# Performance work log

Measured on AMD Instinct MI355X. Metric: run time of the kernel, lower is better.

## Reference

```python
import jax, jax.numpy as jnp
import numpy as np

V, E, H, N, L = 32000, 512, 512, 64, 128


def setup_inputs() -> dict:
    key = jax.random.key(0)
    ks = jax.random.split(key, 16)
    s = 0.02  # init scale
    return {
        "input_ids": jax.random.randint(ks[0], (N,), 0, V),
        "h": jax.random.normal(ks[1], (N, H), jnp.float32),
        "c": jax.random.normal(ks[2], (N, H), jnp.float32),
        "encoder_hiddens": jax.random.normal(ks[3], (N, L, H), jnp.float32),
        "attn_mask": jnp.zeros((N, L), dtype=bool),
        "embed_W": jax.random.normal(ks[4], (V, E), jnp.float32) * s,
        "w_ih": jax.random.normal(ks[5], (4 * H, E), jnp.float32) * s,
        "b_ih": jnp.zeros((4 * H,), jnp.float32),
        "w_hh": jax.random.normal(ks[6], (4 * H, H), jnp.float32) * s,
        "b_hh": jnp.zeros((4 * H,), jnp.float32),
        "attn_Wh": jax.random.normal(ks[7], (H, H), jnp.float32) * s,
        "attn_Ws": jax.random.normal(ks[8], (H, H), jnp.float32) * s,
        "attn_v": jax.random.normal(ks[9], (H,), jnp.float32) * s,
        "h2o_W": jax.random.normal(ks[10], (V, 2 * H), jnp.float32) * s,
        "h2o_b": jnp.zeros((V,), jnp.float32),
    }


def reference(input_ids, h, c, encoder_hiddens, attn_mask, embed_W,
              w_ih, b_ih, w_hh, b_hh, attn_Wh, attn_Ws, attn_v,
              h2o_W, h2o_b):
    # Embedding lookup: (N, E)
    emb = embed_W[input_ids]
    # LSTM cell: fused gate GEMMs, chunk order i, f, g, o (torch chunk(4))
    gates = emb @ w_ih.T + b_ih + h @ w_hh.T + b_hh  # (N, 4H)
    i_g, f_g, g_g, o_g = jnp.split(gates, 4, axis=1)
    c_t = jax.nn.sigmoid(f_g) * c + jax.nn.sigmoid(i_g) * jnp.tanh(g_g)
    h_t = jax.nn.sigmoid(o_g) * jnp.tanh(c_t)  # (N, H)
    # Bahdanau attention: v^T tanh(W_h h_t + W_s enc)
    proj = jnp.tanh((h_t @ attn_Wh.T)[:, None, :] + encoder_hiddens @ attn_Ws.T)  # (N, L, H)
    score = jnp.einsum('nlh,h->nl', proj, attn_v)  # (N, L)
    score = jnp.where(attn_mask, -jnp.inf, score)
    attn_w = jax.nn.softmax(score, axis=1)  # (N, L)
    context = jnp.einsum('nl,nlh->nh', attn_w, encoder_hiddens)  # (N, H)
    # Output projection + log-softmax over vocab
    combined = jnp.concatenate([h_t, context], axis=1)  # (N, 2H)
    out = jax.nn.log_softmax(combined @ h2o_W.T + h2o_b, axis=-1)  # (N, V)
    return out, h_t, c_t
```

## Files before the change

kernel.cpp:

```cpp
#include <hip/hip_runtime.h>
#include <math.h>

#define V 32000
#define E 512
#define H 512
#define N 64
#define L 128
#define NV (N*V)
#define NH (N*H)
#define MTOT (N*L)
#define VT 500

typedef short  s8v  __attribute__((ext_vector_type(8)));
typedef float  f4v  __attribute__((ext_vector_type(4)));

__device__ __forceinline__ float sigf(float x) { return 1.0f / (1.0f + __expf(-x)); }

__device__ __forceinline__ unsigned short f2bf(float f) {
    unsigned int u = __float_as_uint(f);
    unsigned int r = u + 0x7FFFu + ((u >> 16) & 1u);
    return (unsigned short)(r >> 16);
}

__global__ __launch_bounds__(256) void k_gates(
    const int* __restrict__ ids, const float* __restrict__ hprev,
    const float* __restrict__ embW, const float* __restrict__ w_ih,
    const float* __restrict__ w_hh, float* __restrict__ gates_p)
{
    __shared__ __align__(16) float xs[64 * 128];
    const int bx = blockIdx.x;
    const int ks = blockIdx.y;
    const int tid = threadIdx.x;
    const bool emb_part = (ks < 4);
    const int koff = (ks & 3) * 128;

    for (int i = tid; i < 64 * 32; i += 256) {
        int n = i >> 5, kk4 = i & 31;
        float4 x4;
        if (emb_part)
            x4 = ((const float4*)(embW + (size_t)ids[n] * E + koff))[kk4];
        else
            x4 = ((const float4*)(hprev + (size_t)n * H + koff))[kk4];
        ((float4*)xs)[n * 32 + kk4] = x4;
    }
    __syncthreads();

    const int jl = tid & 63;
    const int ng = tid >> 6;
    const int j = bx * 64 + jl;
    const int nb = ng * 16;
    const float* wrow = (emb_part ? w_ih : w_hh) + (size_t)j * 512 + koff;

    float acc[16];
#pragma unroll
    for (int i = 0; i < 16; ++i) acc[i] = 0.f;

    for (int e4 = 0; e4 < 32; ++e4) {
        float4 w4 = ((const float4*)wrow)[e4];
#pragma unroll
        for (int i = 0; i < 16; ++i) {
            float4 x4 = ((const float4*)xs)[(nb + i) * 32 + e4];
            acc[i] += w4.x * x4.x + w4.y * x4.y + w4.z * x4.z + w4.w * x4.w;
        }
    }
#pragma unroll
    for (int i = 0; i < 16; ++i)
        gates_p[(size_t)ks * (64 * 2048) + (size_t)(nb + i) * 2048 + j] = acc[i];
}

__global__ __launch_bounds__(256) void k_lstm_pw(
    const float* __restrict__ gates_p, const float* __restrict__ b_ih,
    const float* __restrict__ b_hh, const float* __restrict__ cprev,
    float* __restrict__ out, unsigned short* __restrict__ xb)
{
    int i = blockIdx.x * 256 + threadIdx.x;
    if (i >= NH) return;
    int n = i >> 9, k = i & 511;
    float g[4];
#pragma unroll
    for (int q = 0; q < 4; ++q) {
        int j = q * 512 + k;
        float s = b_ih[j] + b_hh[j];
#pragma unroll
        for (int ks = 0; ks < 8; ++ks)
            s += gates_p[(size_t)ks * (64 * 2048) + (size_t)n * 2048 + j];
        g[q] = s;
    }
    float ig = sigf(g[0]), fg = sigf(g[1]), gg = tanhf(g[2]), og = sigf(g[3]);
    float ct = fg * cprev[i] + ig * gg;
    float ht = og * tanhf(ct);
    out[NV + i] = ht;
    out[NV + NH + i] = ct;
    xb[(size_t)n * 1024 + k] = f2bf(ht);
}

__global__ __launch_bounds__(256) void k_sproj(
    const float* __restrict__ out, const float* __restrict__ Wh,
    float* __restrict__ sproj)
{
    __shared__ __align__(16) float xs[512];
    int n = blockIdx.x >> 1;
    int h = (blockIdx.x & 1) * 256 + threadIdx.x;
    const float* ht = out + NV + (size_t)n * 512;
    for (int i = threadIdx.x; i < 512; i += 256) xs[i] = ht[i];
    __syncthreads();
    const float* wrow = Wh + (size_t)h * 512;
    float acc = 0.f;
    for (int e4 = 0; e4 < 128; ++e4) {
        float4 w4 = ((const float4*)wrow)[e4];
        float4 x4 = ((const float4*)xs)[e4];
        acc += w4.x * x4.x + w4.y * x4.y + w4.z * x4.z + w4.w * x4.w;
    }
    sproj[(size_t)n * 512 + h] = acc;
}

__global__ __launch_bounds__(256) void k_score_gemm(
    const float* __restrict__ enc, const float* __restrict__ Ws,
    const float* __restrict__ sproj, const float* __restrict__ av,
    float* __restrict__ scorep)
{
    __shared__ __align__(16) short As[64 * 72];
    __shared__ __align__(16) short Bs[64 * 72];
    __shared__ float sred[64];

    const int bm = blockIdx.x, bh = blockIdx.y;
    const int tid = threadIdx.x;
    const int w = tid >> 6, l = tid & 63;
    const int wave_m = (w >> 1) * 32, wave_h = (w & 1) * 32;
    const int lq = l >> 4, lr = l & 15;

    if (tid < 64) sred[tid] = 0.f;

    f4v acc[2][2];
#pragma unroll
    for (int i = 0; i < 2; ++i)
#pragma unroll
        for (int j = 0; j < 2; ++j) acc[i][j] = (f4v)0.f;

    for (int kt = 0; kt < 8; ++kt) {
        __syncthreads();
#pragma unroll
        for (int r = 0; r < 2; ++r) {
            int idx = (r * 256 + tid) * 8;
            int row = idx >> 6, col = idx & 63;
            const float* sa = enc + (size_t)(bm * 64 + row) * 512 + kt * 64 + col;
            const float* sb = Ws  + (size_t)(bh * 64 + row) * 512 + kt * 64 + col;
            float4 a0 = *(const float4*)sa, a1 = *(const float4*)(sa + 4);
            float4 b0 = *(const float4*)sb, b1 = *(const float4*)(sb + 4);
            union { unsigned short u[8]; uint4 q; } pa, pb;
            pa.u[0]=f2bf(a0.x); pa.u[1]=f2bf(a0.y); pa.u[2]=f2bf(a0.z); pa.u[3]=f2bf(a0.w);
            pa.u[4]=f2bf(a1.x); pa.u[5]=f2bf(a1.y); pa.u[6]=f2bf(a1.z); pa.u[7]=f2bf(a1.w);
            pb.u[0]=f2bf(b0.x); pb.u[1]=f2bf(b0.y); pb.u[2]=f2bf(b0.z); pb.u[3]=f2bf(b0.w);
            pb.u[4]=f2bf(b1.x); pb.u[5]=f2bf(b1.y); pb.u[6]=f2bf(b1.z); pb.u[7]=f2bf(b1.w);
            *(uint4*)(As + row * 72 + col) = pa.q;
            *(uint4*)(Bs + row * 72 + col) = pb.q;
        }
        __syncthreads();

#pragma unroll
        for (int ks = 0; ks < 2; ++ks) {
            s8v a_frag[2], b_frag[2];
#pragma unroll
            for (int i = 0; i < 2; ++i)
                a_frag[i] = *(const s8v*)(As + (wave_m + 16 * i + lr) * 72 + ks * 32 + lq * 8);
#pragma unroll
            for (int j = 0; j < 2; ++j)
                b_frag[j] = *(const s8v*)(Bs + (wave_h + 16 * j + lr) * 72 + ks * 32 + lq * 8);
#pragma unroll
            for (int i = 0; i < 2; ++i)
#pragma unroll
                for (int j = 0; j < 2; ++j)
                    acc[i][j] = __builtin_amdgcn_mfma_f32_16x16x32_bf16(
                        a_frag[i], b_frag[j], acc[i][j], 0, 0, 0);
        }
    }
    __syncthreads();

    const int hc0 = bh * 64 + wave_h + lr;
#pragma unroll
    for (int i = 0; i < 2; ++i) {
#pragma unroll
        for (int reg = 0; reg < 4; ++reg) {
            int m_local = wave_m + 16 * i + lq * 4 + reg;
            int m = bm * 64 + m_local;
            int n = m >> 7;
            float p = 0.f;
#pragma unroll
            for (int j = 0; j < 2; ++j) {
                int hc = hc0 + 16 * j;
                float val = acc[i][j][reg] + sproj[(size_t)n * 512 + hc];
                p += tanhf(val) * av[hc];
            }
            p += __shfl_xor(p, 1, 64);
            p += __shfl_xor(p, 2, 64);
            p += __shfl_xor(p, 4, 64);
            p += __shfl_xor(p, 8, 64);
            if (lr == 0) atomicAdd(&sred[m_local], p);
        }
    }
    __syncthreads();
    if (tid < 64)
        scorep[(size_t)bh * MTOT + bm * 64 + tid] = sred[tid];
}

__global__ __launch_bounds__(512) void k_softmax_ctx(
    const float* __restrict__ scorep, const unsigned char* __restrict__ mask,
    const float* __restrict__ enc, unsigned short* __restrict__ xb)
{
    __shared__ float sc[128];
    __shared__ float wl[128];
    const int n = blockIdx.x, t = threadIdx.x;

    if (t < 128) {
        float s = 0.f;
#pragma unroll
        for (int q = 0; q < 8; ++q)
            s += scorep[(size_t)q * MTOT + n * 128 + t];
        if (mask[(size_t)n * 128 + t]) s = -1e30f;
        sc[t] = s;
    }
    __syncthreads();
    if (t < 64) {
        float m = fmaxf(sc[t], sc[t + 64]);
#pragma unroll
        for (int off = 32; off > 0; off >>= 1) m = fmaxf(m, __shfl_xor(m, off, 64));
        float e0 = __expf(sc[t] - m), e1 = __expf(sc[t + 64] - m);
        float ss = e0 + e1;
#pragma unroll
        for (int off = 32; off > 0; off >>= 1) ss += __shfl_xor(ss, off, 64);
        float inv = 1.0f / ss;
        wl[t] = e0 * inv;
        wl[t + 64] = e1 * inv;
    }
    __syncthreads();

    const float* encn = enc + (size_t)n * L * H + t;
    float acc = 0.f;
#pragma unroll 4
    for (int ll = 0; ll < 128; ++ll)
        acc += wl[ll] * encn[(size_t)ll * 512];
    xb[(size_t)n * 1024 + 512 + t] = f2bf(acc);
}

__global__ __launch_bounds__(256) void k_logits(
    const float* __restrict__ h2oW, const unsigned short* __restrict__ xb,
    const float* __restrict__ h2ob, float* __restrict__ dlogits,
    float* __restrict__ pmax, float* __restrict__ psum)
{
    __shared__ __align__(16) short As[64 * 72];
    __shared__ __align__(16) short Bs[64 * 72];
    __shared__ __align__(16) float cs[64 * 68];

    const int bm = blockIdx.x;
    const int tid = threadIdx.x;
    const int w = tid >> 6, l = tid & 63;
    const int wave_m = (w & 1) * 32, wave_n = (w >> 1) * 32;
    const int lq = l >> 4, lr = l & 15;

    const int arow = tid >> 2;
    const int acol = (tid & 3) * 16;
    const float* aptr = h2oW + (size_t)(bm * 64 + arow) * 1024 + acol;
    const unsigned short* bptr = xb + (size_t)arow * 1024 + acol;

    f4v acc[2][2];
#pragma unroll
    for (int i = 0; i < 2; ++i)
#pragma unroll
        for (int j = 0; j < 2; ++j) acc[i][j] = (f4v)0.f;

    float4 ra[4];
    uint4  rb[2];
#pragma unroll
    for (int r = 0; r < 4; ++r) ra[r] = ((const float4*)aptr)[r];
    rb[0] = *(const uint4*)bptr;
    rb[1] = *(const uint4*)(bptr + 8);

#pragma unroll 1
    for (int kt = 0; kt < 16; ++kt) {
        if (kt) __syncthreads();
        union { unsigned short u[8]; uint4 q; } p0, p1;
        p0.u[0]=f2bf(ra[0].x); p0.u[1]=f2bf(ra[0].y); p0.u[2]=f2bf(ra[0].z); p0.u[3]=f2bf(ra[0].w);
        p0.u[4]=f2bf(ra[1].x); p0.u[5]=f2bf(ra[1].y); p0.u[6]=f2bf(ra[1].z); p0.u[7]=f2bf(ra[1].w);
        p1.u[0]=f2bf(ra[2].x); p1.u[1]=f2bf(ra[2].y); p1.u[2]=f2bf(ra[2].z); p1.u[3]=f2bf(ra[2].w);
        p1.u[4]=f2bf(ra[3].x); p1.u[5]=f2bf(ra[3].y); p1.u[6]=f2bf(ra[3].z); p1.u[7]=f2bf(ra[3].w);
        *(uint4*)(As + arow * 72 + acol)     = p0.q;
        *(uint4*)(As + arow * 72 + acol + 8) = p1.q;
        *(uint4*)(Bs + arow * 72 + acol)     = rb[0];
        *(uint4*)(Bs + arow * 72 + acol + 8) = rb[1];
        __syncthreads();

        if (kt < 15) {
            const float* ap = aptr + (kt + 1) * 64;
            const unsigned short* bp = bptr + (kt + 1) * 64;
#pragma unroll
            for (int r = 0; r < 4; ++r) ra[r] = ((const float4*)ap)[r];
            rb[0] = *(const uint4*)bp;
            rb[1] = *(const uint4*)(bp + 8);
        }

#pragma unroll
        for (int ks = 0; ks < 2; ++ks) {
            s8v a_frag[2], b_frag[2];
#pragma unroll
            for (int i = 0; i < 2; ++i)
                a_frag[i] = *(const s8v*)(As + (wave_m + 16 * i + lr) * 72 + ks * 32 + lq * 8);
#pragma unroll
            for (int j = 0; j < 2; ++j)
                b_frag[j] = *(const s8v*)(Bs + (wave_n + 16 * j + lr) * 72 + ks * 32 + lq * 8);
#pragma unroll
            for (int i = 0; i < 2; ++i)
#pragma unroll
                for (int j = 0; j < 2; ++j)
                    acc[i][j] = __builtin_amdgcn_mfma_f32_16x16x32_bf16(
                        a_frag[i], b_frag[j], acc[i][j], 0, 0, 0);
        }
    }
    __syncthreads();

#pragma unroll
    for (int i = 0; i < 2; ++i)
#pragma unroll
        for (int j = 0; j < 2; ++j)
#pragma unroll
            for (int reg = 0; reg < 4; ++reg)
                cs[(wave_n + 16 * j + lr) * 68 + wave_m + 16 * i + lq * 4 + reg] = acc[i][j][reg];
    __syncthreads();

    const int n = tid >> 2, q = tid & 3;
    const int v0 = bm * 64 + q * 16;
    float4 vals[4];
    float m_loc = -1e30f;
#pragma unroll
    for (int k = 0; k < 4; ++k) {
        float4 cv = *(const float4*)(cs + n * 68 + q * 16 + 4 * k);
        float4 bv = *(const float4*)(h2ob + v0 + 4 * k);
        cv.x += bv.x; cv.y += bv.y; cv.z += bv.z; cv.w += bv.w;
        vals[k] = cv;
        *(float4*)(dlogits + (size_t)n * V + v0 + 4 * k) = cv;
        m_loc = fmaxf(m_loc, fmaxf(fmaxf(cv.x, cv.y), fmaxf(cv.z, cv.w)));
    }
    float s_loc = 0.f;
#pragma unroll
    for (int k = 0; k < 4; ++k) {
        s_loc += __expf(vals[k].x - m_loc) + __expf(vals[k].y - m_loc)
               + __expf(vals[k].z - m_loc) + __expf(vals[k].w - m_loc);
    }
    float m2 = fmaxf(m_loc, __shfl_xor(m_loc, 1, 64));
    m2 = fmaxf(m2, __shfl_xor(m2, 2, 64));
    s_loc *= __expf(m_loc - m2);
    float s2 = s_loc + __shfl_xor(s_loc, 1, 64);
    s2 += __shfl_xor(s2, 2, 64);
    if (q == 0) {
        pmax[(size_t)n * VT + bm] = m2;
        psum[(size_t)n * VT + bm] = s2;
    }
}

__global__ __launch_bounds__(256) void k_lse(
    const float* __restrict__ pmax, const float* __restrict__ psum,
    float* __restrict__ lse)
{
    __shared__ float rm[4], rs[4];
    const int n = blockIdx.x, t = threadIdx.x;
    float m0 = (t < VT) ? pmax[(size_t)n * VT + t] : -1e30f;
    float m1 = (t + 256 < VT) ? pmax[(size_t)n * VT + t + 256] : -1e30f;
    float mm = fmaxf(m0, m1);
#pragma unroll
    for (int off = 32; off > 0; off >>= 1) mm = fmaxf(mm, __shfl_xor(mm, off, 64));
    if ((t & 63) == 0) rm[t >> 6] = mm;
    __syncthreads();
    float m = fmaxf(fmaxf(rm[0], rm[1]), fmaxf(rm[2], rm[3]));

    float s = 0.f;
    if (t < VT)       s += psum[(size_t)n * VT + t] * __expf(m0 - m);
    if (t + 256 < VT) s += psum[(size_t)n * VT + t + 256] * __expf(m1 - m);
#pragma unroll
    for (int off = 32; off > 0; off >>= 1) s += __shfl_xor(s, off, 64);
    if ((t & 63) == 0) rs[t >> 6] = s;
    __syncthreads();
    if (t == 0) {
        float st = rs[0] + rs[1] + rs[2] + rs[3];
        lse[n] = m + __logf(st);
    }
}

__global__ __launch_bounds__(256) void k_norm(
    float* __restrict__ dlogits, const float* __restrict__ lse)
{
    const int n = blockIdx.y;
    const int t4 = blockIdx.x * 256 + threadIdx.x;
    if (t4 >= V / 4) return;
    float s = lse[n];
    float4* p = (float4*)(dlogits + (size_t)n * V) + t4;
    float4 v = *p;
    v.x -= s; v.y -= s; v.z -= s; v.w -= s;
    *p = v;
}

extern "C" void kernel_launch(void* const* d_in, const int* in_sizes, int n_in,
                              void* d_out, int out_size, void* d_ws, size_t ws_size,
                              hipStream_t stream)
{
    const int* ids   = (const int*)d_in[0];
    const float* h   = (const float*)d_in[1];
    const float* c   = (const float*)d_in[2];
    const float* enc = (const float*)d_in[3];
    const unsigned char* mask = (const unsigned char*)d_in[4];
    const float* embW = (const float*)d_in[5];
    const float* w_ih = (const float*)d_in[6];
    const float* b_ih = (const float*)d_in[7];
    const float* w_hh = (const float*)d_in[8];
    const float* b_hh = (const float*)d_in[9];
    const float* Wh   = (const float*)d_in[10];
    const float* Ws   = (const float*)d_in[11];
    const float* av   = (const float*)d_in[12];
    const float* h2oW = (const float*)d_in[13];
    const float* h2ob = (const float*)d_in[14];

    float* out = (float*)d_out;
    float* ws = (float*)d_ws;
    float* gates_p = ws;
    float* sproj   = ws + 1048576;
    float* scorep  = ws + 1048576 + 32768;
    unsigned short* xb = (unsigned short*)(ws + 1048576 + 32768 + 65536);
    float* pmax = ws;
    float* psum = ws + 32000;
    float* lse  = ws + 64000;

    k_gates<<<dim3(32, 8), 256, 0, stream>>>(ids, h, embW, w_ih, w_hh, gates_p);
    k_lstm_pw<<<128, 256, 0, stream>>>(gates_p, b_ih, b_hh, c, out, xb);
    k_sproj<<<128, 256, 0, stream>>>(out, Wh, sproj);
    k_score_gemm<<<dim3(128, 8), 256, 0, stream>>>(enc, Ws, sproj, av, scorep);
    k_softmax_ctx<<<64, 512, 0, stream>>>(scorep, mask, enc, xb);
    k_logits<<<VT, 256, 0, stream>>>(h2oW, xb, h2ob, out, pmax, psum);
    k_lse<<<64, 256, 0, stream>>>(pmax, psum, lse);
    k_norm<<<dim3(32, 64), 256, 0, stream>>>(out, lse);
}
```

Before: 348.9 us.

## Split-K logits GEMM, wider softmax-ctx grid, packed bf16 convert, swapped score grid

The logits kernel now uses 512 threads in two groups, each handling half of K with its own LDS tiles, and their partial accumulators are summed in shared memory. The register prefetch of the next tile is dropped. The softmax/context kernel is spread over a 64x4 grid of 128-thread blocks, and the score GEMM grid is transposed so consecutive blocks share an encoder tile. Scalar float-to-bf16 rounding is replaced with the paired __float22bfloat162_rn conversion. The aim is more parallelism per block and cheaper conversions, at the cost of losing load/compute overlap in the logits GEMM and adding an extra reduction step.

After: 342.4 us. Within noise of the previous version (-1.9%).

```diff
diff --git a/kernel.cpp b/kernel.cpp
--- a/kernel.cpp
+++ b/kernel.cpp
@@ -1,4 +1,5 @@
 #include <hip/hip_runtime.h>
+#include <hip/hip_bf16.h>
 #include <math.h>
 
 #define V 32000
@@ -22,6 +23,20 @@
     return (unsigned short)(r >> 16);
 }
 
+__device__ __forceinline__ unsigned int cvt2bf(float x, float y) {
+    __hip_bfloat162 h2 = __float22bfloat162_rn(make_float2(x, y));
+    unsigned int r;
+    __builtin_memcpy(&r, &h2, 4);
+    return r;
+}
+
+__device__ __forceinline__ uint4 pack_q(float4 lo, float4 hi) {
+    uint4 q;
+    q.x = cvt2bf(lo.x, lo.y); q.y = cvt2bf(lo.z, lo.w);
+    q.z = cvt2bf(hi.x, hi.y); q.w = cvt2bf(hi.z, hi.w);
+    return q;
+}
+
 __global__ __launch_bounds__(256) void k_gates(
     const int* __restrict__ ids, const float* __restrict__ hprev,
     const float* __restrict__ embW, const float* __restrict__ w_ih,
@@ -123,7 +138,7 @@
     __shared__ __align__(16) short Bs[64 * 72];
     __shared__ float sred[64];
 
-    const int bm = blockIdx.x, bh = blockIdx.y;
+    const int bh = blockIdx.x, bm = blockIdx.y;
     const int tid = threadIdx.x;
     const int w = tid >> 6, l = tid & 63;
     const int wave_m = (w >> 1) * 32, wave_h = (w & 1) * 32;
@@ -147,13 +162,8 @@
             const float* sb = Ws  + (size_t)(bh * 64 + row) * 512 + kt * 64 + col;
             float4 a0 = *(const float4*)sa, a1 = *(const float4*)(sa + 4);
             float4 b0 = *(const float4*)sb, b1 = *(const float4*)(sb + 4);
-            union { unsigned short u[8]; uint4 q; } pa, pb;
-            pa.u[0]=f2bf(a0.x); pa.u[1]=f2bf(a0.y); pa.u[2]=f2bf(a0.z); pa.u[3]=f2bf(a0.w);
-            pa.u[4]=f2bf(a1.x); pa.u[5]=f2bf(a1.y); pa.u[6]=f2bf(a1.z); pa.u[7]=f2bf(a1.w);
-            pb.u[0]=f2bf(b0.x); pb.u[1]=f2bf(b0.y); pb.u[2]=f2bf(b0.z); pb.u[3]=f2bf(b0.w);
-            pb.u[4]=f2bf(b1.x); pb.u[5]=f2bf(b1.y); pb.u[6]=f2bf(b1.z); pb.u[7]=f2bf(b1.w);
-            *(uint4*)(As + row * 72 + col) = pa.q;
-            *(uint4*)(Bs + row * 72 + col) = pb.q;
+            *(uint4*)(As + row * 72 + col) = pack_q(a0, a1);
+            *(uint4*)(Bs + row * 72 + col) = pack_q(b0, b1);
         }
         __syncthreads();
 
@@ -203,64 +213,69 @@
         scorep[(size_t)bh * MTOT + bm * 64 + tid] = sred[tid];
 }
 
-__global__ __launch_bounds__(512) void k_softmax_ctx(
+__global__ __launch_bounds__(128) void k_softmax_ctx(
     const float* __restrict__ scorep, const unsigned char* __restrict__ mask,
     const float* __restrict__ enc, unsigned short* __restrict__ xb)
 {
-    __shared__ float sc[128];
     __shared__ float wl[128];
-    const int n = blockIdx.x, t = threadIdx.x;
-
-    if (t < 128) {
-        float s = 0.f;
-#pragma unroll
-        for (int q = 0; q < 8; ++q)
-            s += scorep[(size_t)q * MTOT + n * 128 + t];
-        if (mask[(size_t)n * 128 + t]) s = -1e30f;
-        sc[t] = s;
-    }
-    __syncthreads();
-    if (t < 64) {
-        float m = fmaxf(sc[t], sc[t + 64]);
-#pragma unroll
-        for (int off = 32; off > 0; off >>= 1) m = fmaxf(m, __shfl_xor(m, off, 64));
-        float e0 = __expf(sc[t] - m), e1 = __expf(sc[t + 64] - m);
-        float ss = e0 + e1;
-#pragma unroll
-        for (int off = 32; off > 0; off >>= 1) ss += __shfl_xor(ss, off, 64);
-        float inv = 1.0f / ss;
-        wl[t] = e0 * inv;
-        wl[t + 64] = e1 * inv;
-    }
-    __syncthreads();
-
-    const float* encn = enc + (size_t)n * L * H + t;
+    __shared__ float red[4];
+    const int n = blockIdx.x, hc = blockIdx.y, t = threadIdx.x;
+
+    float s = 0.f;
+#pragma unroll
+    for (int q = 0; q < 8; ++q)
+        s += scorep[(size_t)q * MTOT + n * 128 + t];
+    if (mask[(size_t)n * 128 + t]) s = -1e30f;
+
+    float m = s;
+#pragma unroll
+    for (int off = 32; off > 0; off >>= 1) m = fmaxf(m, __shfl_xor(m, off, 64));
+    if ((t & 63) == 0) red[t >> 6] = m;
+    __syncthreads();
+    m = fmaxf(red[0], red[1]);
+    float e = __expf(s - m);
+    float ss = e;
+#pragma unroll
+    for (int off = 32; off > 0; off >>= 1) ss += __shfl_xor(ss, off, 64);
+    if ((t & 63) == 0) red[2 + (t >> 6)] = ss;
+    __syncthreads();
+    float inv = 1.0f / (red[2] + red[3]);
+    wl[t] = e * inv;
+    __syncthreads();
+
+    const float* encn = enc + (size_t)n * (L * H) + hc * 128 + t;
     float acc = 0.f;
-#pragma unroll 4
+#pragma unroll 8
     for (int ll = 0; ll < 128; ++ll)
         acc += wl[ll] * encn[(size_t)ll * 512];
-    xb[(size_t)n * 1024 + 512 + t] = f2bf(acc);
-}
-
-__global__ __launch_bounds__(256) void k_logits(
+    xb[(size_t)n * 1024 + 512 + hc * 128 + t] = f2bf(acc);
+}
+
+__global__ __launch_bounds__(512) void k_logits(
     const float* __restrict__ h2oW, const unsigned short* __restrict__ xb,
     const float* __restrict__ h2ob, float* __restrict__ dlogits,
     float* __restrict__ pmax, float* __restrict__ psum)
 {
-    __shared__ __align__(16) short As[64 * 72];
-    __shared__ __align__(16) short Bs[64 * 72];
+    __shared__ __align__(16) short As[2][64 * 72];
+    __shared__ __align__(16) short Bs[2][64 * 72];
     __shared__ __align__(16) float cs[64 * 68];
 
     const int bm = blockIdx.x;
     const int tid = threadIdx.x;
-    const int w = tid >> 6, l = tid & 63;
-    const int wave_m = (w & 1) * 32, wave_n = (w >> 1) * 32;
+    const int g = tid >> 8;
+    const int tl = tid & 255;
+    const int w2 = (tid >> 6) & 3;
+    const int l = tid & 63;
+    const int wave_m = (w2 & 1) * 32, wave_n = (w2 >> 1) * 32;
     const int lq = l >> 4, lr = l & 15;
 
-    const int arow = tid >> 2;
-    const int acol = (tid & 3) * 16;
-    const float* aptr = h2oW + (size_t)(bm * 64 + arow) * 1024 + acol;
-    const unsigned short* bptr = xb + (size_t)arow * 1024 + acol;
+    const int arow = tl >> 2;
+    const int acol = (tl & 3) * 16;
+    const float* aptr = h2oW + (size_t)(bm * 64 + arow) * 1024 + g * 512 + acol;
+    const unsigned short* bptr = xb + (size_t)arow * 1024 + g * 512 + acol;
+
+    short* Asg = As[g];
+    short* Bsg = Bs[g];
 
     f4v acc[2][2];
 #pragma unroll
@@ -268,45 +283,29 @@
 #pragma unroll
         for (int j = 0; j < 2; ++j) acc[i][j] = (f4v)0.f;
 
-    float4 ra[4];
-    uint4  rb[2];
-#pragma unroll
-    for (int r = 0; r < 4; ++r) ra[r] = ((const float4*)aptr)[r];
-    rb[0] = *(const uint4*)bptr;
-    rb[1] = *(const uint4*)(bptr + 8);
-
 #pragma unroll 1
-    for (int kt = 0; kt < 16; ++kt) {
+    for (int kt = 0; kt < 8; ++kt) {
         if (kt) __syncthreads();
-        union { unsigned short u[8]; uint4 q; } p0, p1;
-        p0.u[0]=f2bf(ra[0].x); p0.u[1]=f2bf(ra[0].y); p0.u[2]=f2bf(ra[0].z); p0.u[3]=f2bf(ra[0].w);
-        p0.u[4]=f2bf(ra[1].x); p0.u[5]=f2bf(ra[1].y); p0.u[6]=f2bf(ra[1].z); p0.u[7]=f2bf(ra[1].w);
-        p1.u[0]=f2bf(ra[2].x); p1.u[1]=f2bf(ra[2].y); p1.u[2]=f2bf(ra[2].z); p1.u[3]=f2bf(ra[2].w);
-        p1.u[4]=f2bf(ra[3].x); p1.u[5]=f2bf(ra[3].y); p1.u[6]=f2bf(ra[3].z); p1.u[7]=f2bf(ra[3].w);
-        *(uint4*)(As + arow * 72 + acol)     = p0.q;
-        *(uint4*)(As + arow * 72 + acol + 8) = p1.q;
-        *(uint4*)(Bs + arow * 72 + acol)     = rb[0];
-        *(uint4*)(Bs + arow * 72 + acol + 8) = rb[1];
+        const float* ap = aptr + kt * 64;
+        const unsigned short* bp = bptr + kt * 64;
+        float4 a0 = ((const float4*)ap)[0], a1 = ((const float4*)ap)[1];
+        float4 a2 = ((const float4*)ap)[2], a3 = ((const float4*)ap)[3];
+        uint4 b0 = *(const uint4*)bp, b1 = *(const uint4*)(bp + 8);
+        *(uint4*)(Asg + arow * 72 + acol)     = pack_q(a0, a1);
+        *(uint4*)(Asg + arow * 72 + acol + 8) = pack_q(a2, a3);
+        *(uint4*)(Bsg + arow * 72 + acol)     = b0;
+        *(uint4*)(Bsg + arow * 72 + acol + 8) = b1;
         __syncthreads();
-
-        if (kt < 15) {
-            const float* ap = aptr + (kt + 1) * 64;
-            const unsigned short* bp = bptr + (kt + 1) * 64;
-#pragma unroll
-            for (int r = 0; r < 4; ++r) ra[r] = ((const float4*)ap)[r];
-            rb[0] = *(const uint4*)bp;
-            rb[1] = *(const uint4*)(bp + 8);
-        }
 
 #pragma unroll
         for (int ks = 0; ks < 2; ++ks) {
             s8v a_frag[2], b_frag[2];
 #pragma unroll
             for (int i = 0; i < 2; ++i)
-                a_frag[i] = *(const s8v*)(As + (wave_m + 16 * i + lr) * 72 + ks * 32 + lq * 8);
+                a_frag[i] = *(const s8v*)(Asg + (wave_m + 16 * i + lr) * 72 + ks * 32 + lq * 8);
 #pragma unroll
             for (int j = 0; j < 2; ++j)
-                b_frag[j] = *(const s8v*)(Bs + (wave_n + 16 * j + lr) * 72 + ks * 32 + lq * 8);
+                b_frag[j] = *(const s8v*)(Bsg + (wave_n + 16 * j + lr) * 72 + ks * 32 + lq * 8);
 #pragma unroll
             for (int i = 0; i < 2; ++i)
 #pragma unroll
@@ -317,42 +316,56 @@
     }
     __syncthreads();
 
-#pragma unroll
-    for (int i = 0; i < 2; ++i)
-#pragma unroll
-        for (int j = 0; j < 2; ++j)
-#pragma unroll
-            for (int reg = 0; reg < 4; ++reg)
-                cs[(wave_n + 16 * j + lr) * 68 + wave_m + 16 * i + lq * 4 + reg] = acc[i][j][reg];
-    __syncthreads();
-
-    const int n = tid >> 2, q = tid & 3;
-    const int v0 = bm * 64 + q * 16;
-    float4 vals[4];
-    float m_loc = -1e30f;
-#pragma unroll
-    for (int k = 0; k < 4; ++k) {
-        float4 cv = *(const float4*)(cs + n * 68 + q * 16 + 4 * k);
-        float4 bv = *(const float4*)(h2ob + v0 + 4 * k);
-        cv.x += bv.x; cv.y += bv.y; cv.z += bv.z; cv.w += bv.w;
-        vals[k] = cv;
-        *(float4*)(dlogits + (size_t)n * V + v0 + 4 * k) = cv;
-        m_loc = fmaxf(m_loc, fmaxf(fmaxf(cv.x, cv.y), fmaxf(cv.z, cv.w)));
-    }
-    float s_loc = 0.f;
-#pragma unroll
-    for (int k = 0; k < 4; ++k) {
-        s_loc += __expf(vals[k].x - m_loc) + __expf(vals[k].y - m_loc)
-               + __expf(vals[k].z - m_loc) + __expf(vals[k].w - m_loc);
-    }
-    float m2 = fmaxf(m_loc, __shfl_xor(m_loc, 1, 64));
-    m2 = fmaxf(m2, __shfl_xor(m2, 2, 64));
-    s_loc *= __expf(m_loc - m2);
-    float s2 = s_loc + __shfl_xor(s_loc, 1, 64);
-    s2 += __shfl_xor(s2, 2, 64);
-    if (q == 0) {
-        pmax[(size_t)n * VT + bm] = m2;
-        psum[(size_t)n * VT + bm] = s2;
+    if (g == 0) {
+#pragma unroll
+        for (int i = 0; i < 2; ++i)
+#pragma unroll
+            for (int j = 0; j < 2; ++j)
+#pragma unroll
+                for (int reg = 0; reg < 4; ++reg)
+                    cs[(wave_n + 16 * j + lr) * 68 + wave_m + 16 * i + lq * 4 + reg] = acc[i][j][reg];
+    }
+    __syncthreads();
+    if (g == 1) {
+#pragma unroll
+        for (int i = 0; i < 2; ++i)
+#pragma unroll
+            for (int j = 0; j < 2; ++j)
+#pragma unroll
+                for (int reg = 0; reg < 4; ++reg)
+                    cs[(wave_n + 16 * j + lr) * 68 + wave_m + 16 * i + lq * 4 + reg] += acc[i][j][reg];
+    }
+    __syncthreads();
+
+    if (tid < 256) {
+        const int n = tid >> 2, q = tid & 3;
+        const int v0 = bm * 64 + q * 16;
+        float4 vals[4];
+        float m_loc = -1e30f;
+#pragma unroll
+        for (int k = 0; k < 4; ++k) {
+            float4 cv = *(const float4*)(cs + n * 68 + q * 16 + 4 * k);
+            float4 bv = *(const float4*)(h2ob + v0 + 4 * k);
+            cv.x += bv.x; cv.y += bv.y; cv.z += bv.z; cv.w += bv.w;
+            vals[k] = cv;
+            *(float4*)(dlogits + (size_t)n * V + v0 + 4 * k) = cv;
+            m_loc = fmaxf(m_loc, fmaxf(fmaxf(cv.x, cv.y), fmaxf(cv.z, cv.w)));
+        }
+        float s_loc = 0.f;
+#pragma unroll
+        for (int k = 0; k < 4; ++k) {
+            s_loc += __expf(vals[k].x - m_loc) + __expf(vals[k].y - m_loc)
+                   + __expf(vals[k].z - m_loc) + __expf(vals[k].w - m_loc);
+        }
+        float m2 = fmaxf(m_loc, __shfl_xor(m_loc, 1, 64));
+        m2 = fmaxf(m2, __shfl_xor(m2, 2, 64));
+        s_loc *= __expf(m_loc - m2);
+        float s2 = s_loc + __shfl_xor(s_loc, 1, 64);
+        s2 += __shfl_xor(s2, 2, 64);
+        if (q == 0) {
+            pmax[(size_t)n * VT + bm] = m2;
+            psum[(size_t)n * VT + bm] = s2;
+        }
     }
 }
 
@@ -430,9 +443,9 @@
     k_gates<<<dim3(32, 8), 256, 0, stream>>>(ids, h, embW, w_ih, w_hh, gates_p);
     k_lstm_pw<<<128, 256, 0, stream>>>(gates_p, b_ih, b_hh, c, out, xb);
     k_sproj<<<128, 256, 0, stream>>>(out, Wh, sproj);
-    k_score_gemm<<<dim3(128, 8), 256, 0, stream>>>(enc, Ws, sproj, av, scorep);
-    k_softmax_ctx<<<64, 512, 0, stream>>>(scorep, mask, enc, xb);
-    k_logits<<<VT, 256, 0, stream>>>(h2oW, xb, h2ob, out, pmax, psum);
+    k_score_gemm<<<dim3(8, 128), 256, 0, stream>>>(enc, Ws, sproj, av, scorep);
+    k_softmax_ctx<<<dim3(64, 4), 128, 0, stream>>>(scorep, mask, enc, xb);
+    k_logits<<<VT, 512, 0, stream>>>(h2oW, xb, h2ob, out, pmax, psum);
     k_lse<<<64, 256, 0, stream>>>(pmax, psum, lse);
     k_norm<<<dim3(32, 64), 256, 0, stream>>>(out, lse);
 }
```
